# Kernel optimization log

Hardware: AMD Instinct MI355X
Metric: run time of the kernel (lower is better)

## Reference

```python
import jax, jax.numpy as jnp
import numpy as np

NODES_PER_GRAPH = 21
NUM_GRAPHS = 50000
N = NODES_PER_GRAPH * NUM_GRAPHS  # 1,050,000 nodes
NUM_FEATURES = 3
NUM_CLASSES = 29
H1, H2 = 64, 128
BN_EPS = 1e-5

_HAND = np.array([(0, 1), (1, 2), (2, 3), (3, 4), (0, 5), (5, 6), (6, 7), (7, 8),
                  (0, 9), (9, 10), (10, 11), (11, 12), (0, 13), (13, 14), (14, 15),
                  (15, 16), (0, 17), (17, 18), (18, 19), (19, 20)], dtype=np.int64).T  # [2,20]


def setup_inputs() -> dict:
    key = jax.random.key(0)
    ks = jax.random.split(key, 16)
    # Tile hand skeleton across NUM_GRAPHS disjoint graphs with node offsets.
    offsets = (np.arange(NUM_GRAPHS, dtype=np.int64) * NODES_PER_GRAPH)  # [G]
    ei = (_HAND[:, None, :] + offsets[None, :, None]).reshape(2, -1)      # [2, G*20]
    edge_index = jnp.asarray(ei)
    batch = jnp.asarray(np.repeat(np.arange(NUM_GRAPHS, dtype=np.int64), NODES_PER_GRAPH))

    x = jax.random.normal(ks[0], (N, NUM_FEATURES), dtype=jnp.float32)

    def lin(k, fi, fo):
        kw, kb = jax.random.split(k)
        s = 1.0 / np.sqrt(fi)
        return (jax.random.uniform(kw, (fi, fo), jnp.float32, -s, s),
                jax.random.uniform(kb, (fo,), jnp.float32, -s, s))

    W1, b1 = lin(ks[1], NUM_FEATURES, H1)
    W2, b2 = lin(ks[2], H1, H2)
    W3, b3 = lin(ks[3], H2, NUM_CLASSES)

    def bn(k, d):
        k1, k2, k3, k4 = jax.random.split(k, 4)
        return (1.0 + 0.1 * jax.random.normal(k1, (d,), jnp.float32),   # gamma
                0.1 * jax.random.normal(k2, (d,), jnp.float32),          # beta
                0.01 * jax.random.normal(k3, (d,), jnp.float32),         # running_mean
                jax.random.uniform(k4, (d,), jnp.float32, 0.5, 1.5))     # running_var

    g1, be1, m1, v1 = bn(ks[4], H1)
    g2, be2, m2, v2 = bn(ks[5], H2)

    return {"x": x, "W1": W1, "b1": b1, "g1": g1, "be1": be1, "m1": m1, "v1": v1,
            "W2": W2, "b2": b2, "g2": g2, "be2": be2, "m2": m2, "v2": v2,
            "W3": W3, "b3": b3, "edge_index": edge_index, "batch": batch}


def gcn_conv(x, W, b, src, dst):
    """PyG GCNConv: linear, add self-loops, sym-normalized scatter-add, bias."""
    h = x @ W                                              # [N, Fout]
    deg = jnp.zeros((N,), x.dtype).at[dst].add(1.0) + 1.0  # in-degree incl. self-loop
    dinv = deg ** -0.5
    msg = h[src] * (dinv[src] * dinv[dst])[:, None]        # edge-wise gather + normalize
    out = jnp.zeros_like(h).at[dst].add(msg)               # scatter-add aggregation
    out = out + h * (dinv * dinv)[:, None]                 # self-loop contribution
    return out + b


def bn_eval(x, gamma, beta, mean, var):
    return (x - mean) * (gamma * jax.lax.rsqrt(var + BN_EPS)) + beta


def reference(x, W1, b1, g1, be1, m1, v1, W2, b2, g2, be2, m2, v2, W3, b3,
              edge_index, batch):
    src, dst = edge_index[0], edge_index[1]
    h = jax.nn.relu(bn_eval(gcn_conv(x, W1, b1, src, dst), g1, be1, m1, v1))
    # dropout is identity in eval mode
    h = jax.nn.relu(bn_eval(gcn_conv(h, W2, b2, src, dst), g2, be2, m2, v2))
    h = gcn_conv(h, W3, b3, src, dst)                      # [N, C]
    summed = jax.ops.segment_sum(h, batch, num_segments=NUM_GRAPHS)
    counts = jax.ops.segment_sum(jnp.ones((N,), h.dtype), batch, num_segments=NUM_GRAPHS)
    pooled = summed / counts[:, None]                      # global mean pool [G, C]
    return jax.nn.log_softmax(pooled, axis=1)
```

## Files before the change

### kernel.cpp

```cpp
#include <hip/hip_runtime.h>
#include <math.h>


#define G_TOTAL 50000
#define NPG 21
#define GPB 6
#define NCHUNK ((G_TOTAL + GPB - 1) / GPB)
#define NCLS 29
#define BN_EPS 1e-5f
#define INV_SQRT2 0.70710678118654752440f
#define ROOT_COLSUM 4.53553390593273762f

#define WS_W1B  0
#define WS_B2   256
#define WS_B3   384
#define WS_W3T  416
#define WS_BF   4128
#define WS_TOTAL (WS_BF + 4096)

typedef short s16x8 __attribute__((ext_vector_type(8)));
typedef float f32x4 __attribute__((ext_vector_type(4)));

__device__ __forceinline__ unsigned f2bf_rne(float f) {
    unsigned u = __float_as_uint(f);
    return (u + 0x7FFFu + ((u >> 16) & 1u)) >> 16;
}

__global__ void prep_kernel(const float* __restrict__ W1, const float* __restrict__ b1,
                            const float* __restrict__ g1, const float* __restrict__ be1,
                            const float* __restrict__ m1, const float* __restrict__ v1,
                            const float* __restrict__ W2, const float* __restrict__ b2,
                            const float* __restrict__ g2, const float* __restrict__ be2,
                            const float* __restrict__ m2, const float* __restrict__ v2,
                            const float* __restrict__ W3, const float* __restrict__ b3,
                            float* __restrict__ ws) {
    int t = blockIdx.x * blockDim.x + threadIdx.x;
    if (t < 256) {
        int k = t >> 2, comp = t & 3;
        float s = g1[k] * rsqrtf(v1[k] + BN_EPS);
        float v;
        if (comp < 3) v = W1[comp * 64 + k] * s;
        else          v = (b1[k] - m1[k]) * s + be1[k];
        ws[WS_W1B + t] = v;
    } else if (t < 384) {
        int j = t - 256;
        float s = g2[j] * rsqrtf(v2[j] + BN_EPS);
        ws[WS_B2 + j] = (b2[j] - m2[j]) * s + be2[j];
    } else if (t < 416) {
        int j = t - 384;
        ws[WS_B3 + j] = (j < NCLS) ? b3[j] : 0.f;
    } else if (t < WS_BF) {
        int i = t - WS_W3T;
        if (i < 3712) {
            int c = i >> 7, k = i & 127;
            ws[WS_W3T + i] = W3[k * NCLS + c];
        }
    } else if (t < WS_TOTAL) {
        int i = t - WS_BF;
        int d  = i & 3;
        int l  = (i >> 2) & 63;
        int ss = (i >> 8) & 1;
        int n  = i >> 9;
        int kg = l >> 4, r = l & 15;
        int c = 16 * n + r;
        float sc = g2[c] * rsqrtf(v2[c] + BN_EPS);
        int k0 = 32 * ss + 8 * kg + 2 * d;
        unsigned h0 = f2bf_rne(W2[k0 * 128 + c] * sc);
        unsigned h1 = f2bf_rne(W2[(k0 + 1) * 128 + c] * sc);
        ((unsigned*)ws)[WS_BF + i] = (h1 << 16) | h0;
    }
}

__global__ __launch_bounds__(256, 4)
void gcn_main(const float* __restrict__ x, const float* __restrict__ ws,
              float* __restrict__ out) {
    __shared__ __align__(16) float sZ[8704];
    __shared__ __align__(16) float4 sW1B[64];
    __shared__ float  sb2[128];
    __shared__ __align__(8) float2 sLUT[128];
    __shared__ float  sP[GPB * 128];

    const int tid = threadIdx.x;
    const int g0 = blockIdx.x * GPB;
    const int nv = min(GPB, G_TOTAL - g0);
    const int Mrows = nv * NPG;

    if (tid < 64) sW1B[tid] = ((const float4*)ws)[tid];
    else if (tid < 192) sb2[tid - 64] = ws[WS_B2 + (tid - 64)];
    if (tid < 128) {
        const int r = tid;
        const int lg2 = (r * 3121) >> 16;
        const int j = r - NPG * lg2;
        float w = (j == 0) ? (ROOT_COLSUM / 21.f)
                           : (((j & 3) == 0) ? (0.5f / 21.f) : (1.f / 21.f));
        if (r >= Mrows) w = 0.f;
        sLUT[r] = make_float2(w, (float)lg2);
    }
    __syncthreads();

    const int node = tid >> 1;
    const int s = tid & 1;
    const int k0 = s * 32;
    const int lg = (node * 3121) >> 16;
    const int j21 = node - NPG * lg;
    float z[32];
    {
        const int dist = (j21 == 0) ? 0 : (((j21 & 3) == 1) ? j21 : 1);
        const float c = ((j21 & 3) == 1) ? INV_SQRT2 : 0.5f;
        float s0 = 0.f, s1 = 0.f, s2 = 0.f, q0 = 0.f, q1 = 0.f, q2 = 0.f;
        if (node < Mrows) {
            const long long gid = (long long)(g0 + lg) * NPG + j21;
            const float* xp = x + gid * 3;
            s0 = xp[0]; s1 = xp[1]; s2 = xp[2];
            const float* xq = xp - dist * 3;
            q0 = xq[0]; q1 = xq[1]; q2 = xq[2];
        }
        const float ax0 = fmaf(c, q0, 0.5f * s0);
        const float ax1 = fmaf(c, q1, 0.5f * s1);
        const float ax2 = fmaf(c, q2, 0.5f * s2);
        #pragma unroll
        for (int kk = 0; kk < 32; ++kk) {
            const float4 wv = sW1B[k0 + kk];
            float t = fmaf(ax0, wv.x, wv.w);
            t = fmaf(ax1, wv.y, t);
            t = fmaf(ax2, wv.z, t);
            z[kk] = fmaxf(t, 0.f);
        }
        #pragma unroll
        for (int q = 0; q < 8; ++q)
            *(float4*)&sZ[node * 68 + k0 + 4 * q] =
                make_float4(z[4*q], z[4*q+1], z[4*q+2], z[4*q+3]);
    }
    __syncthreads();

    {
        const int dist = (j21 == 0) ? 0 : (((j21 & 3) == 1) ? j21 : 1);
        const float c = ((j21 & 3) == 1) ? INV_SQRT2 : 0.5f;
        const int prow = node - dist;
        #pragma unroll
        for (int q = 0; q < 8; ++q) {
            const float4 zp = *(const float4*)&sZ[prow * 68 + k0 + 4 * q];
            z[4*q]   = fmaf(c, zp.x, 0.5f * z[4*q]);
            z[4*q+1] = fmaf(c, zp.y, 0.5f * z[4*q+1]);
            z[4*q+2] = fmaf(c, zp.z, 0.5f * z[4*q+2]);
            z[4*q+3] = fmaf(c, zp.w, 0.5f * z[4*q+3]);
        }
    }
    __syncthreads();

    {
        unsigned dw[16];
        #pragma unroll
        for (int p = 0; p < 16; ++p)
            dw[p] = __builtin_amdgcn_perm(__float_as_uint(z[2*p+1]),
                                          __float_as_uint(z[2*p]), 0x07060302u);
        char* fragB = (char*)sZ + ((node >> 4) * 2 + s) * 1024 + (node & 15) * 16;
        #pragma unroll
        for (int g = 0; g < 4; ++g)
            *(uint4*)(fragB + g * 256) =
                make_uint4(dw[4*g], dw[4*g+1], dw[4*g+2], dw[4*g+3]);
    }
    __syncthreads();

    {
        const int w = tid >> 6;
        const int lane = tid & 63;
        const int r = lane & 15;
        const int g4 = lane >> 4;
        const uint4* wsB = (const uint4*)((const unsigned*)ws + WS_BF);
        uint4 B00 = wsB[((2*w+0)*2 + 0)*64 + lane];
        uint4 B01 = wsB[((2*w+0)*2 + 1)*64 + lane];
        uint4 B10 = wsB[((2*w+1)*2 + 0)*64 + lane];
        uint4 B11 = wsB[((2*w+1)*2 + 1)*64 + lane];
        const float b2c0 = sb2[32*w + r];
        const float b2c1 = sb2[32*w + 16 + r];
        const float2* lutp = &sLUT[4 * g4];
        const char* fragB = (const char*)sZ + lane * 16;

        float pg[GPB][2];
        #pragma unroll
        for (int g = 0; g < GPB; ++g) { pg[g][0] = 0.f; pg[g][1] = 0.f; }

        #pragma unroll
        for (int m = 0; m < 8; ++m) {
            const s16x8 A0 = *(const s16x8*)(fragB + (2*m + 0) * 1024);
            const s16x8 A1 = *(const s16x8*)(fragB + (2*m + 1) * 1024);
            f32x4 acc0 = {0.f, 0.f, 0.f, 0.f};
            f32x4 acc1 = {0.f, 0.f, 0.f, 0.f};
            acc0 = __builtin_amdgcn_mfma_f32_16x16x32_bf16(A0, *(const s16x8*)&B00, acc0, 0, 0, 0);
            acc0 = __builtin_amdgcn_mfma_f32_16x16x32_bf16(A1, *(const s16x8*)&B01, acc0, 0, 0, 0);
            acc1 = __builtin_amdgcn_mfma_f32_16x16x32_bf16(A0, *(const s16x8*)&B10, acc1, 0, 0, 0);
            acc1 = __builtin_amdgcn_mfma_f32_16x16x32_bf16(A1, *(const s16x8*)&B11, acc1, 0, 0, 0);

            #pragma unroll
            for (int i = 0; i < 4; ++i) {
                const float2 wg = lutp[16*m + i];
                const float t0 = fmaxf(acc0[i] + b2c0, 0.f) * wg.x;
                const float t1 = fmaxf(acc1[i] + b2c1, 0.f) * wg.x;
                const int lo = (16*m + i) / 21;
                const int hiRaw = (16*m + i + 12) / 21;
                const int hi = (hiRaw > 5) ? 5 : hiRaw;
                if (lo == hiRaw) {
                    pg[lo][0] += t0; pg[lo][1] += t1;
                } else {
                    const bool cA = (wg.y == (float)lo);
                    const float s0 = cA ? t0 : 0.f;
                    const float s1 = cA ? t1 : 0.f;
                    pg[lo][0] += s0; pg[hi][0] += t0 - s0;
                    pg[lo][1] += s1; pg[hi][1] += t1 - s1;
                }
            }
        }
        #pragma unroll
        for (int g = 0; g < GPB; ++g) {
            #pragma unroll
            for (int c = 0; c < 2; ++c) {
                float v = pg[g][c];
                v += __shfl_xor(v, 16);
                v += __shfl_xor(v, 32);
                pg[g][c] = v;
            }
        }
        if (lane < 16) {
            #pragma unroll
            for (int g = 0; g < GPB; ++g) {
                sP[g * 128 + 32*w + r]      = pg[g][0];
                sP[g * 128 + 32*w + 16 + r] = pg[g][1];
            }
        }
    }
    __syncthreads();

    float* sLg = sZ;
    float* sRed = sZ + 192;
    if (tid < GPB * NCLS) {
        const int g = (tid * 2260) >> 16;
        const int c = tid - g * NCLS;
        const float4* w3 = (const float4*)(ws + WS_W3T + c * 128);
        const float4* pp = (const float4*)&sP[g * 128];
        float acc3 = ws[WS_B3 + c];
        #pragma unroll
        for (int k = 0; k < 32; ++k) {
            const float4 wv = w3[k];
            const float4 pv = pp[k];
            acc3 = fmaf(pv.x, wv.x, acc3);
            acc3 = fmaf(pv.y, wv.y, acc3);
            acc3 = fmaf(pv.z, wv.z, acc3);
            acc3 = fmaf(pv.w, wv.w, acc3);
        }
        sLg[tid] = acc3;
    }
    __syncthreads();
    if (tid < nv) {
        float m = -1e30f;
        for (int c = 0; c < NCLS; ++c) m = fmaxf(m, sLg[tid * NCLS + c]);
        float sum = 0.f;
        for (int c = 0; c < NCLS; ++c) sum += expf(sLg[tid * NCLS + c] - m);
        sRed[tid * 2] = m;
        sRed[tid * 2 + 1] = logf(sum);
    }
    __syncthreads();
    if (tid < nv * NCLS) {
        const int g = (tid * 2260) >> 16;
        out[(long long)g0 * NCLS + tid] = sLg[tid] - sRed[g * 2] - sRed[g * 2 + 1];
    }
}

extern "C" void kernel_launch(void* const* d_in, const int* in_sizes, int n_in,
                              void* d_out, int out_size, void* d_ws, size_t ws_size,
                              hipStream_t stream) {
    const float* x   = (const float*)d_in[0];
    const float* W1  = (const float*)d_in[1];
    const float* b1  = (const float*)d_in[2];
    const float* g1  = (const float*)d_in[3];
    const float* be1 = (const float*)d_in[4];
    const float* m1  = (const float*)d_in[5];
    const float* v1  = (const float*)d_in[6];
    const float* W2  = (const float*)d_in[7];
    const float* b2  = (const float*)d_in[8];
    const float* g2  = (const float*)d_in[9];
    const float* be2 = (const float*)d_in[10];
    const float* m2  = (const float*)d_in[11];
    const float* v2  = (const float*)d_in[12];
    const float* W3  = (const float*)d_in[13];
    const float* b3  = (const float*)d_in[14];
    float* out = (float*)d_out;
    float* ws  = (float*)d_ws;

    prep_kernel<<<(WS_TOTAL + 255) / 256, 256, 0, stream>>>(
        W1, b1, g1, be1, m1, v1, W2, b2, g2, be2, m2, v2, W3, b3, ws);

    gcn_main<<<NCHUNK, 256, 0, stream>>>(x, ws, out);
}
```

Measured before the change: 220.6 us.

## Shrink LDS via bf16 fragment reuse, stage x in LDS, warp-shuffle log-softmax

The fp32 intermediate buffer (sZ, 8704 floats) is dropped. The layer-1 neighbour aggregation now reads the neighbour's bf16 values from the MFMA fragment buffer, which is written twice. This cuts LDS per block so more blocks fit on a CU (launch bounds raised from 4 to 7). The x rows are loaded coalesced into LDS instead of being gathered per thread. Log-softmax now uses wave shuffles instead of a serial per-graph loop, which removes one barrier. The neighbour is rounded to bf16 before aggregation, which may slightly change accuracy.

```diff
diff --git a/kernel.cpp b/kernel.cpp
--- a/kernel.cpp
+++ b/kernel.cpp
@@ -71,14 +71,14 @@
     }
 }
 
-__global__ __launch_bounds__(256, 4)
+__global__ __launch_bounds__(256, 7)
 void gcn_main(const float* __restrict__ x, const float* __restrict__ ws,
               float* __restrict__ out) {
-    __shared__ __align__(16) float sZ[8704];
+    __shared__ __align__(16) float sFrag[4096];
     __shared__ __align__(16) float4 sW1B[64];
-    __shared__ float  sb2[128];
+    __shared__ float sb2[128];
     __shared__ __align__(8) float2 sLUT[128];
-    __shared__ float  sP[GPB * 128];
+    __shared__ __align__(16) float sP[GPB * 128];
 
     const int tid = threadIdx.x;
     const int g0 = blockIdx.x * GPB;
@@ -96,6 +96,11 @@
         if (r >= Mrows) w = 0.f;
         sLUT[r] = make_float2(w, (float)lg2);
     }
+    {
+        const int n2 = (Mrows * 3) >> 1;
+        const float2* xg2 = (const float2*)(x + (long long)g0 * 63);
+        if (tid < n2) ((float2*)sP)[tid] = xg2[tid];
+    }
     __syncthreads();
 
     const int node = tid >> 1;
@@ -103,21 +108,17 @@
     const int k0 = s * 32;
     const int lg = (node * 3121) >> 16;
     const int j21 = node - NPG * lg;
+    const int dist = (j21 == 0) ? 0 : (((j21 & 3) == 1) ? j21 : 1);
+    const float cw = ((j21 & 3) == 1) ? INV_SQRT2 : 0.5f;
+    char* const fragB = (char*)sFrag + ((node >> 4) * 2 + s) * 1024 + (node & 15) * 16;
     float z[32];
     {
-        const int dist = (j21 == 0) ? 0 : (((j21 & 3) == 1) ? j21 : 1);
-        const float c = ((j21 & 3) == 1) ? INV_SQRT2 : 0.5f;
-        float s0 = 0.f, s1 = 0.f, s2 = 0.f, q0 = 0.f, q1 = 0.f, q2 = 0.f;
-        if (node < Mrows) {
-            const long long gid = (long long)(g0 + lg) * NPG + j21;
-            const float* xp = x + gid * 3;
-            s0 = xp[0]; s1 = xp[1]; s2 = xp[2];
-            const float* xq = xp - dist * 3;
-            q0 = xq[0]; q1 = xq[1]; q2 = xq[2];
-        }
-        const float ax0 = fmaf(c, q0, 0.5f * s0);
-        const float ax1 = fmaf(c, q1, 0.5f * s1);
-        const float ax2 = fmaf(c, q2, 0.5f * s2);
+        const float* xs = (const float*)sP + node * 3;
+        const float s0 = xs[0], s1 = xs[1], s2 = xs[2];
+        const float* xq = xs - dist * 3;
+        const float ax0 = fmaf(cw, xq[0], 0.5f * s0);
+        const float ax1 = fmaf(cw, xq[1], 0.5f * s1);
+        const float ax2 = fmaf(cw, xq[2], 0.5f * s2);
         #pragma unroll
         for (int kk = 0; kk < 32; ++kk) {
             const float4 wv = sW1B[k0 + kk];
@@ -126,35 +127,43 @@
             t = fmaf(ax2, wv.z, t);
             z[kk] = fmaxf(t, 0.f);
         }
-        #pragma unroll
-        for (int q = 0; q < 8; ++q)
-            *(float4*)&sZ[node * 68 + k0 + 4 * q] =
-                make_float4(z[4*q], z[4*q+1], z[4*q+2], z[4*q+3]);
-    }
-    __syncthreads();
-
-    {
-        const int dist = (j21 == 0) ? 0 : (((j21 & 3) == 1) ? j21 : 1);
-        const float c = ((j21 & 3) == 1) ? INV_SQRT2 : 0.5f;
-        const int prow = node - dist;
-        #pragma unroll
-        for (int q = 0; q < 8; ++q) {
-            const float4 zp = *(const float4*)&sZ[prow * 68 + k0 + 4 * q];
-            z[4*q]   = fmaf(c, zp.x, 0.5f * z[4*q]);
-            z[4*q+1] = fmaf(c, zp.y, 0.5f * z[4*q+1]);
-            z[4*q+2] = fmaf(c, zp.z, 0.5f * z[4*q+2]);
-            z[4*q+3] = fmaf(c, zp.w, 0.5f * z[4*q+3]);
-        }
-    }
-    __syncthreads();
-
-    {
         unsigned dw[16];
         #pragma unroll
         for (int p = 0; p < 16; ++p)
             dw[p] = __builtin_amdgcn_perm(__float_as_uint(z[2*p+1]),
                                           __float_as_uint(z[2*p]), 0x07060302u);
-        char* fragB = (char*)sZ + ((node >> 4) * 2 + s) * 1024 + (node & 15) * 16;
+        #pragma unroll
+        for (int g = 0; g < 4; ++g)
+            *(uint4*)(fragB + g * 256) =
+                make_uint4(dw[4*g], dw[4*g+1], dw[4*g+2], dw[4*g+3]);
+    }
+    __syncthreads();
+
+    if (dist != 0) {
+        const int prow = node - dist;
+        const char* pfrag = (const char*)sFrag
+                          + ((prow >> 4) * 2 + s) * 1024 + (prow & 15) * 16;
+        #pragma unroll
+        for (int g = 0; g < 4; ++g) {
+            const uint4 pd = *(const uint4*)(pfrag + g * 256);
+            const unsigned d4[4] = {pd.x, pd.y, pd.z, pd.w};
+            #pragma unroll
+            for (int d = 0; d < 4; ++d) {
+                const float plo = __uint_as_float(d4[d] << 16);
+                const float phi = __uint_as_float(d4[d] & 0xFFFF0000u);
+                z[8*g + 2*d]     = fmaf(cw, plo, 0.5f * z[8*g + 2*d]);
+                z[8*g + 2*d + 1] = fmaf(cw, phi, 0.5f * z[8*g + 2*d + 1]);
+            }
+        }
+    }
+    __syncthreads();
+
+    {
+        unsigned dw[16];
+        #pragma unroll
+        for (int p = 0; p < 16; ++p)
+            dw[p] = __builtin_amdgcn_perm(__float_as_uint(z[2*p+1]),
+                                          __float_as_uint(z[2*p]), 0x07060302u);
         #pragma unroll
         for (int g = 0; g < 4; ++g)
             *(uint4*)(fragB + g * 256) =
@@ -175,7 +184,7 @@
         const float b2c0 = sb2[32*w + r];
         const float b2c1 = sb2[32*w + 16 + r];
         const float2* lutp = &sLUT[4 * g4];
-        const char* fragB = (const char*)sZ + lane * 16;
+        const char* fragA = (const char*)sFrag + lane * 16;
 
         float pg[GPB][2];
         #pragma unroll
@@ -183,8 +192,8 @@
 
         #pragma unroll
         for (int m = 0; m < 8; ++m) {
-            const s16x8 A0 = *(const s16x8*)(fragB + (2*m + 0) * 1024);
-            const s16x8 A1 = *(const s16x8*)(fragB + (2*m + 1) * 1024);
+            const s16x8 A0 = *(const s16x8*)(fragA + (2*m + 0) * 1024);
+            const s16x8 A1 = *(const s16x8*)(fragA + (2*m + 1) * 1024);
             f32x4 acc0 = {0.f, 0.f, 0.f, 0.f};
             f32x4 acc1 = {0.f, 0.f, 0.f, 0.f};
             acc0 = __builtin_amdgcn_mfma_f32_16x16x32_bf16(A0, *(const s16x8*)&B00, acc0, 0, 0, 0);
@@ -231,8 +240,7 @@
     }
     __syncthreads();
 
-    float* sLg = sZ;
-    float* sRed = sZ + 192;
+    float* sLg = sFrag;
     if (tid < GPB * NCLS) {
         const int g = (tid * 2260) >> 16;
         const int c = tid - g * NCLS;
@@ -251,18 +259,26 @@
         sLg[tid] = acc3;
     }
     __syncthreads();
-    if (tid < nv) {
-        float m = -1e30f;
-        for (int c = 0; c < NCLS; ++c) m = fmaxf(m, sLg[tid * NCLS + c]);
-        float sum = 0.f;
-        for (int c = 0; c < NCLS; ++c) sum += expf(sLg[tid * NCLS + c] - m);
-        sRed[tid * 2] = m;
-        sRed[tid * 2 + 1] = logf(sum);
-    }
-    __syncthreads();
-    if (tid < nv * NCLS) {
-        const int g = (tid * 2260) >> 16;
-        out[(long long)g0 * NCLS + tid] = sLg[tid] - sRed[g * 2] - sRed[g * 2 + 1];
+
+    if (tid < 192) {
+        const int g = tid >> 5, c = tid & 31;
+        const bool act = (c < NCLS) && (g < nv);
+        float v = act ? sLg[g * NCLS + c] : -1e30f;
+        float m = v;
+        m = fmaxf(m, __shfl_xor(m, 1));
+        m = fmaxf(m, __shfl_xor(m, 2));
+        m = fmaxf(m, __shfl_xor(m, 4));
+        m = fmaxf(m, __shfl_xor(m, 8));
+        m = fmaxf(m, __shfl_xor(m, 16));
+        float e = act ? expf(v - m) : 0.f;
+        float ss = e;
+        ss += __shfl_xor(ss, 1);
+        ss += __shfl_xor(ss, 2);
+        ss += __shfl_xor(ss, 4);
+        ss += __shfl_xor(ss, 8);
+        ss += __shfl_xor(ss, 16);
+        if (act)
+            out[(long long)g0 * NCLS + g * NCLS + c] = v - m - logf(ss);
     }
 }
 
```

After: 200.9 us. 8.9% less time.
